# Kernel optimization log

Hardware: AMD Instinct MI355X
Metric: run time of the kernel (lower is better)

The kernel has to match this reference:

```python
import jax, jax.numpy as jnp
import numpy as np

LEAK = 0.95
THRESHOLD = 1.0
RESCALE = 2.0


def _xavier_uniform(key, shape, gain=2.0):
    fan_out, fan_in = shape
    bound = gain * np.sqrt(6.0 / (fan_in + fan_out))
    return jax.random.uniform(key, shape, jnp.float32, -bound, bound)


def setup_inputs() -> dict:
    key = jax.random.key(0)
    k_inp, k_w1, k_w2 = jax.random.split(key, 3)
    inp = jax.random.normal(k_inp, (8192, 784), jnp.float32)
    w1 = _xavier_uniform(k_w1, (800, 784))   # fc1.weight
    w2 = _xavier_uniform(k_w2, (10, 800))    # fc2.weight
    return {"inp": inp, "w1": w1, "w2": w2, "num_steps": 25}


@jax.custom_vjp
def spike_fn(x):
    return (x > 0).astype(x.dtype)

def _spike_fwd(x):
    return spike_fn(x), x

def _spike_bwd(x, g):
    # grad = g * 0.3 * relu(1 - |x|)  (surrogate BP)
    return (g * 0.3 * jnp.maximum(1.0 - jnp.abs(x), 0.0),)

spike_fn.defvjp(_spike_fwd, _spike_bwd)


def poisson_gen(key, inp):
    r = jax.random.uniform(key, inp.shape, inp.dtype)
    temp = (r * RESCALE <= jnp.abs(inp)).astype(inp.dtype) * jnp.sign(inp)
    return 0.5 * (temp + 1.0)


def reference(inp, w1, w2, num_steps):
    batch = inp.shape[0]
    x = inp.reshape(batch, -1)
    keys = jax.random.split(jax.random.key(42), num_steps)

    def step(carry, key):
        mem1, mem2 = carry
        sp = poisson_gen(key, x)                    # [B, 784]
        mem1 = LEAK * mem1 + (1.0 - LEAK) * (sp @ w1.T)  # [B, 800]
        mem_thr = mem1 / THRESHOLD - 1.0
        out = spike_fn(mem_thr)
        rst = jnp.where(mem_thr > 0, THRESHOLD, 0.0)
        mem1 = mem1 - jax.lax.stop_gradient(rst)
        mem2 = mem2 + out @ w2.T                    # [B, 10]
        return (mem1, mem2), None

    init = (jnp.zeros((batch, 800), x.dtype), jnp.zeros((batch, 10), x.dtype))
    (_, mem2), _ = jax.lax.scan(step, init, keys)
    return mem2 / num_steps
```

## Files before the change

kernel.cpp:

```cpp
#include <hip/hip_runtime.h>
#include <cstdint>

__host__ __device__ inline uint32_t tf_rotl32(uint32_t x, uint32_t r) {
  return (x << r) | (x >> (32u - r));
}

__host__ __device__ inline void threefry2x32(uint32_t k0, uint32_t k1,
                                             uint32_t x0, uint32_t x1,
                                             uint32_t* o0, uint32_t* o1) {
  uint32_t ks0 = k0, ks1 = k1, ks2 = k0 ^ k1 ^ 0x1BD11BDAu;
  x0 += ks0; x1 += ks1;
#define TF_R(r) { x0 += x1; x1 = tf_rotl32(x1, r); x1 ^= x0; }
  TF_R(13) TF_R(15) TF_R(26) TF_R(6)
  x0 += ks1; x1 += ks2 + 1u;
  TF_R(17) TF_R(29) TF_R(16) TF_R(24)
  x0 += ks2; x1 += ks0 + 2u;
  TF_R(13) TF_R(15) TF_R(26) TF_R(6)
  x0 += ks0; x1 += ks1 + 3u;
  TF_R(17) TF_R(29) TF_R(16) TF_R(24)
  x0 += ks1; x1 += ks2 + 4u;
  TF_R(13) TF_R(15) TF_R(26) TF_R(6)
  x0 += ks2; x1 += ks0 + 5u;
#undef TF_R
  *o0 = x0; *o1 = x1;
}

#define BSZ   8192
#define KIN   784
#define HID   800
#define NOUT  10
#define NSTEP 25

#define PANEL1 264
#define PANEL2 528

__global__ __launch_bounds__(256) void enc_kernel(const float* __restrict__ inp,
                                                  uint8_t* __restrict__ enc,
                                                  uint32_t k0, uint32_t k1) {
  int j = blockIdx.x * blockDim.x + threadIdx.x;
  if (j >= BSZ * KIN) return;
  uint32_t o0, o1;
  threefry2x32(k0, k1, 0u, (uint32_t)j, &o0, &o1);
  uint32_t bits = o0 ^ o1;
  float r = __uint_as_float((bits >> 9) | 0x3f800000u) - 1.0f;
  float x = inp[j];
  bool cond = (2.0f * r <= fabsf(x));
  int s = (x > 0.0f) ? 1 : ((x < 0.0f) ? -1 : 0);
  enc[j] = (uint8_t)(1 + (cond ? s : 0));
}

#define BM 128
#define BN 32
#define BK 16
#define NTILE (KIN / BK)

typedef float f32x2 __attribute__((ext_vector_type(2)));

__device__ __forceinline__ float cvt_ub(uint32_t x, int i) {
  return (float)((x >> (8 * i)) & 0xffu);
}

__device__ __forceinline__ void pk_fma_lo(f32x2& acc, f32x2 a, f32x2 b) {
  asm("v_pk_fma_f32 %0, %1, %2, %0 op_sel:[0,0,0] op_sel_hi:[0,1,1]"
      : "+v"(acc)
      : "v"(a), "v"(b));
}
__device__ __forceinline__ void pk_fma_hi(f32x2& acc, f32x2 a, f32x2 b) {
  asm("v_pk_fma_f32 %0, %1, %2, %0 op_sel:[1,0,0] op_sel_hi:[1,1,1]"
      : "+v"(acc)
      : "v"(a), "v"(b));
}

__global__ __launch_bounds__(256) void gemm_kernel(const uint8_t* __restrict__ enc,
                                                   const float* __restrict__ w1,
                                                   float* __restrict__ g) {
  __shared__ uint32_t As[2][BK][BM / 4];
  __shared__ float    Bs[2][BK][BN];
  const int m0 = blockIdx.x * BM;
  const int n0 = blockIdx.y * BN;
  const int t  = threadIdx.x;

  const int tm = t / 8;
  const int tn = t % 8;

  const bool isA = (t < 128);
  const int u    = t & 127;
  const int ar0  = (u & 31) * 4;
  const int ak0  = (u >> 5) * 4;
  const int brow = u & 31;
  const int bk0  = (u >> 5) * 4;

  const uint8_t* aptr = enc + (size_t)(m0 + ar0) * KIN + ak0;
  const float*   bptr = w1 + (size_t)(n0 + brow) * KIN + bk0;

  uint32_t rA0, rA1, rA2, rA3;
  float4 rB;

  f32x2 acc[4][2];
  f32x2 tot[4][2];
#pragma unroll
  for (int mi = 0; mi < 4; mi++)
#pragma unroll
    for (int nj = 0; nj < 2; nj++) acc[mi][nj] = (f32x2)(0.0f);

#define LOAD_TILE(K0G)                                               \
  if (isA) {                                                         \
    const uint8_t* ap = aptr + (K0G);                                \
    rA0 = *(const uint32_t*)(ap + (size_t)0 * KIN);                  \
    rA1 = *(const uint32_t*)(ap + (size_t)1 * KIN);                  \
    rA2 = *(const uint32_t*)(ap + (size_t)2 * KIN);                  \
    rA3 = *(const uint32_t*)(ap + (size_t)3 * KIN);                  \
  } else {                                                           \
    rB = *(const float4*)(bptr + (K0G));                             \
  }

#define STORE_TILE(P)                                                \
  if (isA) {                                                         \
    uint32_t a01  = __builtin_amdgcn_perm(rA1, rA0, 0x05010400u);    \
    uint32_t a01h = __builtin_amdgcn_perm(rA1, rA0, 0x07030602u);    \
    uint32_t a23  = __builtin_amdgcn_perm(rA3, rA2, 0x05010400u);    \
    uint32_t a23h = __builtin_amdgcn_perm(rA3, rA2, 0x07030602u);    \
    As[P][ak0 + 0][ar0 >> 2] = __builtin_amdgcn_perm(a23,  a01,  0x05040100u); \
    As[P][ak0 + 1][ar0 >> 2] = __builtin_amdgcn_perm(a23,  a01,  0x07060302u); \
    As[P][ak0 + 2][ar0 >> 2] = __builtin_amdgcn_perm(a23h, a01h, 0x05040100u); \
    As[P][ak0 + 3][ar0 >> 2] = __builtin_amdgcn_perm(a23h, a01h, 0x07060302u); \
  } else {                                                           \
    Bs[P][bk0 + 0][brow] = rB.x;                                     \
    Bs[P][bk0 + 1][brow] = rB.y;                                     \
    Bs[P][bk0 + 2][brow] = rB.z;                                     \
    Bs[P][bk0 + 3][brow] = rB.w;                                     \
  }

  LOAD_TILE(0)
  STORE_TILE(0)
  __syncthreads();

  int p = 0;
  for (int tile = 0; tile < NTILE; tile++) {
    const int kbase = tile * BK;
    const bool more = (tile + 1 < NTILE);
    if (more) { LOAD_TILE(kbase + BK) }
#pragma unroll
    for (int kk = 0; kk < BK; kk++) {
      const int kglob = kbase + kk;
      if (kglob == PANEL1) {
#pragma unroll
        for (int mi = 0; mi < 4; mi++)
#pragma unroll
          for (int nj = 0; nj < 2; nj++) {
            tot[mi][nj] = acc[mi][nj];
            acc[mi][nj] = (f32x2)(0.0f);
          }
      } else if (kglob == PANEL2) {
#pragma unroll
        for (int mi = 0; mi < 4; mi++)
#pragma unroll
          for (int nj = 0; nj < 2; nj++) {
            tot[mi][nj].x = __fadd_rn(tot[mi][nj].x, acc[mi][nj].x);
            tot[mi][nj].y = __fadd_rn(tot[mi][nj].y, acc[mi][nj].y);
            acc[mi][nj] = (f32x2)(0.0f);
          }
      }
      uint32_t aw = As[p][kk][tm];
      f32x2 am[2];
      am[0].x = cvt_ub(aw, 0);
      am[0].y = cvt_ub(aw, 1);
      am[1].x = cvt_ub(aw, 2);
      am[1].y = cvt_ub(aw, 3);
      float4 bv = *(const float4*)&Bs[p][kk][tn * 4];
      f32x2 b2[2];
      b2[0].x = bv.x; b2[0].y = bv.y;
      b2[1].x = bv.z; b2[1].y = bv.w;
#pragma unroll
      for (int mp = 0; mp < 2; mp++) {
        pk_fma_lo(acc[2 * mp + 0][0], am[mp], b2[0]);
        pk_fma_lo(acc[2 * mp + 0][1], am[mp], b2[1]);
        pk_fma_hi(acc[2 * mp + 1][0], am[mp], b2[0]);
        pk_fma_hi(acc[2 * mp + 1][1], am[mp], b2[1]);
      }
    }
    if (more) { STORE_TILE(p ^ 1) }
    __syncthreads();
    p ^= 1;
  }
#undef LOAD_TILE
#undef STORE_TILE

#pragma unroll
  for (int mi = 0; mi < 4; mi++) {
    float* dst = g + (size_t)(m0 + tm * 4 + mi) * HID + n0 + tn * 4;
    float4 o;
    o.x = __fmul_rn(0.5f, __fadd_rn(tot[mi][0].x, acc[mi][0].x));
    o.y = __fmul_rn(0.5f, __fadd_rn(tot[mi][0].y, acc[mi][0].y));
    o.z = __fmul_rn(0.5f, __fadd_rn(tot[mi][1].x, acc[mi][1].x));
    o.w = __fmul_rn(0.5f, __fadd_rn(tot[mi][1].y, acc[mi][1].y));
    *(float4*)dst = o;
  }
}

__global__ __launch_bounds__(256) void update_kernel(const float* __restrict__ g,
                                                     float* __restrict__ mem1,
                                                     const float* __restrict__ w2,
                                                     float* __restrict__ mem2) {
  __shared__ float w2s[NOUT * HID];
  for (int i = threadIdx.x; i < NOUT * HID; i += 256) w2s[i] = w2[i];
  __syncthreads();

  const int wave = threadIdx.x / 64;
  const int lane = threadIdx.x % 64;
  const int b = blockIdx.x * 4 + wave;

  const float* grow = g + (size_t)b * HID;
  float* mrow = mem1 + (size_t)b * HID;

  float acc[NOUT];
#pragma unroll
  for (int i = 0; i < NOUT; i++) acc[i] = 0.0f;

  for (int j = lane; j < HID; j += 64) {
    float m = __fadd_rn(__fmul_rn(0.95f, mrow[j]), __fmul_rn(0.05f, grow[j]));
    bool spike = __fadd_rn(m, -1.0f) > 0.0f;
    mrow[j] = spike ? __fadd_rn(m, -1.0f) : m;
    if (spike) {
#pragma unroll
      for (int i = 0; i < NOUT; i++) acc[i] += w2s[i * HID + j];
    }
  }
#pragma unroll
  for (int i = 0; i < NOUT; i++) {
    float v = acc[i];
    for (int off = 32; off > 0; off >>= 1) v += __shfl_down(v, off);
    if (lane == 0) mem2[(size_t)b * NOUT + i] += v;
  }
}

__global__ __launch_bounds__(256) void finalize_kernel(const float* __restrict__ mem2,
                                                       const int* __restrict__ ns,
                                                       float* __restrict__ out) {
  int i = blockIdx.x * blockDim.x + threadIdx.x;
  if (i < BSZ * NOUT) out[i] = mem2[i] / (float)(*ns);
}

extern "C" void kernel_launch(void* const* d_in, const int* in_sizes, int n_in,
                              void* d_out, int out_size, void* d_ws, size_t ws_size,
                              hipStream_t stream) {
  const float* inp = (const float*)d_in[0];
  const float* w1  = (const float*)d_in[1];
  const float* w2  = (const float*)d_in[2];
  const int*   dns = (const int*)d_in[3];
  float* out = (float*)d_out;

  char* ws = (char*)d_ws;
  size_t off = 0;
  uint8_t* enc = (uint8_t*)(ws + off);  off += (size_t)BSZ * KIN;
  off = (off + 255) & ~(size_t)255;
  float* g    = (float*)(ws + off);     off += (size_t)BSZ * HID * 4;
  float* mem1 = (float*)(ws + off);     off += (size_t)BSZ * HID * 4;
  float* mem2 = (float*)(ws + off);     off += (size_t)BSZ * NOUT * 4;

  (void)hipMemsetAsync(mem1, 0, (size_t)BSZ * HID * 4, stream);
  (void)hipMemsetAsync(mem2, 0, (size_t)BSZ * NOUT * 4, stream);

  uint32_t keys[NSTEP][2];
  for (int t = 0; t < NSTEP; t++)
    threefry2x32(0u, 42u, 0u, (uint32_t)t, &keys[t][0], &keys[t][1]);

  const int n_elem = BSZ * KIN;
  for (int t = 0; t < NSTEP; t++) {
    enc_kernel<<<(n_elem + 255) / 256, 256, 0, stream>>>(inp, enc, keys[t][0], keys[t][1]);
    gemm_kernel<<<dim3(BSZ / BM, HID / BN), 256, 0, stream>>>(enc, w1, g);
    update_kernel<<<BSZ / 4, 256, 0, stream>>>(g, mem1, w2, mem2);
  }
  finalize_kernel<<<(BSZ * NOUT + 255) / 256, 256, 0, stream>>>(mem2, dns, out);
}
```

Before: 4.754 ms.

## Split GEMM K dimension into three panels across grid z and reduce in update

The GEMM now launches three times as many blocks, each covering one of three K panels (264/264/256) with BK reduced to 8. Each block writes its partial sums to a separate buffer, and the update kernel adds the three partials and applies the 0.5 scale. This keeps the same panel summation order as the old kernel, which chained the panels sequentially inside one block, while exposing more parallelism. The cost is triple the intermediate write and read traffic (about 26 MB per partial per step) and smaller K tiles with more barriers per element.

```diff
diff --git a/kernel.cpp b/kernel.cpp
--- a/kernel.cpp
+++ b/kernel.cpp
@@ -31,8 +31,6 @@
 #define NOUT  10
 #define NSTEP 25
 
-#define PANEL1 264
-#define PANEL2 528
 
 __global__ __launch_bounds__(256) void enc_kernel(const float* __restrict__ inp,
                                                   uint8_t* __restrict__ enc,
@@ -51,8 +49,7 @@
 
 #define BM 128
 #define BN 32
-#define BK 16
-#define NTILE (KIN / BK)
+#define BK 8
 
 typedef float f32x2 __attribute__((ext_vector_type(2)));
 
@@ -73,9 +70,12 @@
 
 __global__ __launch_bounds__(256) void gemm_kernel(const uint8_t* __restrict__ enc,
                                                    const float* __restrict__ w1,
-                                                   float* __restrict__ g) {
+                                                   float* __restrict__ gp) {
   __shared__ uint32_t As[2][BK][BM / 4];
   __shared__ float    Bs[2][BK][BN];
+  const int panel  = blockIdx.z;
+  const int kstart = (panel == 0) ? 0 : ((panel == 1) ? 264 : 528);
+  const int ntile  = (panel == 2) ? 32 : 33;
   const int m0 = blockIdx.x * BM;
   const int n0 = blockIdx.y * BN;
   const int t  = threadIdx.x;
@@ -83,52 +83,56 @@
   const int tm = t / 8;
   const int tn = t % 8;
 
-  const bool isA = (t < 128);
-  const int u    = t & 127;
-  const int ar0  = (u & 31) * 4;
-  const int ak0  = (u >> 5) * 4;
-  const int brow = u & 31;
-  const int bk0  = (u >> 5) * 4;
-
-  const uint8_t* aptr = enc + (size_t)(m0 + ar0) * KIN + ak0;
-  const float*   bptr = w1 + (size_t)(n0 + brow) * KIN + bk0;
+  const bool stA = (t < 64);
+  const bool stB = (t >= 128 && t < 192);
+  const int ar0 = (t & 31) * 4;
+  const int ak0 = ((t >> 5) & 1) * 4;
+  const int ub   = (t - 128) & 63;
+  const int brow = ub & 31;
+  const int bk0  = (ub >> 5) * 4;
+
+  const uint8_t* aptr = enc + (size_t)(m0 + ar0) * KIN + kstart + ak0;
+  const float*   bptr = w1 + (size_t)(n0 + brow) * KIN + kstart + bk0;
 
   uint32_t rA0, rA1, rA2, rA3;
   float4 rB;
 
   f32x2 acc[4][2];
-  f32x2 tot[4][2];
 #pragma unroll
   for (int mi = 0; mi < 4; mi++)
 #pragma unroll
     for (int nj = 0; nj < 2; nj++) acc[mi][nj] = (f32x2)(0.0f);
 
-#define LOAD_TILE(K0G)                                               \
-  if (isA) {                                                         \
-    const uint8_t* ap = aptr + (K0G);                                \
-    rA0 = *(const uint32_t*)(ap + (size_t)0 * KIN);                  \
-    rA1 = *(const uint32_t*)(ap + (size_t)1 * KIN);                  \
-    rA2 = *(const uint32_t*)(ap + (size_t)2 * KIN);                  \
-    rA3 = *(const uint32_t*)(ap + (size_t)3 * KIN);                  \
-  } else {                                                           \
-    rB = *(const float4*)(bptr + (K0G));                             \
+#define LOAD_TILE(KOFF)                                              \
+  {                                                                  \
+    if (stA) {                                                       \
+      const uint8_t* ap = aptr + (KOFF);                             \
+      rA0 = *(const uint32_t*)(ap + (size_t)0 * KIN);                \
+      rA1 = *(const uint32_t*)(ap + (size_t)1 * KIN);                \
+      rA2 = *(const uint32_t*)(ap + (size_t)2 * KIN);                \
+      rA3 = *(const uint32_t*)(ap + (size_t)3 * KIN);                \
+    }                                                                \
+    if (stB) rB = *(const float4*)(bptr + (KOFF));                   \
   }
 
 #define STORE_TILE(P)                                                \
-  if (isA) {                                                         \
-    uint32_t a01  = __builtin_amdgcn_perm(rA1, rA0, 0x05010400u);    \
-    uint32_t a01h = __builtin_amdgcn_perm(rA1, rA0, 0x07030602u);    \
-    uint32_t a23  = __builtin_amdgcn_perm(rA3, rA2, 0x05010400u);    \
-    uint32_t a23h = __builtin_amdgcn_perm(rA3, rA2, 0x07030602u);    \
-    As[P][ak0 + 0][ar0 >> 2] = __builtin_amdgcn_perm(a23,  a01,  0x05040100u); \
-    As[P][ak0 + 1][ar0 >> 2] = __builtin_amdgcn_perm(a23,  a01,  0x07060302u); \
-    As[P][ak0 + 2][ar0 >> 2] = __builtin_amdgcn_perm(a23h, a01h, 0x05040100u); \
-    As[P][ak0 + 3][ar0 >> 2] = __builtin_amdgcn_perm(a23h, a01h, 0x07060302u); \
-  } else {                                                           \
-    Bs[P][bk0 + 0][brow] = rB.x;                                     \
-    Bs[P][bk0 + 1][brow] = rB.y;                                     \
-    Bs[P][bk0 + 2][brow] = rB.z;                                     \
-    Bs[P][bk0 + 3][brow] = rB.w;                                     \
+  {                                                                  \
+    if (stA) {                                                       \
+      uint32_t a01  = __builtin_amdgcn_perm(rA1, rA0, 0x05010400u);  \
+      uint32_t a01h = __builtin_amdgcn_perm(rA1, rA0, 0x07030602u);  \
+      uint32_t a23  = __builtin_amdgcn_perm(rA3, rA2, 0x05010400u);  \
+      uint32_t a23h = __builtin_amdgcn_perm(rA3, rA2, 0x07030602u);  \
+      As[P][ak0 + 0][ar0 >> 2] = __builtin_amdgcn_perm(a23,  a01,  0x05040100u); \
+      As[P][ak0 + 1][ar0 >> 2] = __builtin_amdgcn_perm(a23,  a01,  0x07060302u); \
+      As[P][ak0 + 2][ar0 >> 2] = __builtin_amdgcn_perm(a23h, a01h, 0x05040100u); \
+      As[P][ak0 + 3][ar0 >> 2] = __builtin_amdgcn_perm(a23h, a01h, 0x07060302u); \
+    }                                                                \
+    if (stB) {                                                       \
+      Bs[P][bk0 + 0][brow] = rB.x;                                   \
+      Bs[P][bk0 + 1][brow] = rB.y;                                   \
+      Bs[P][bk0 + 2][brow] = rB.z;                                   \
+      Bs[P][bk0 + 3][brow] = rB.w;                                   \
+    }                                                                \
   }
 
   LOAD_TILE(0)
@@ -136,47 +140,29 @@
   __syncthreads();
 
   int p = 0;
-  for (int tile = 0; tile < NTILE; tile++) {
-    const int kbase = tile * BK;
-    const bool more = (tile + 1 < NTILE);
-    if (more) { LOAD_TILE(kbase + BK) }
-#pragma unroll
-    for (int kk = 0; kk < BK; kk++) {
-      const int kglob = kbase + kk;
-      if (kglob == PANEL1) {
-#pragma unroll
-        for (int mi = 0; mi < 4; mi++)
-#pragma unroll
-          for (int nj = 0; nj < 2; nj++) {
-            tot[mi][nj] = acc[mi][nj];
-            acc[mi][nj] = (f32x2)(0.0f);
-          }
-      } else if (kglob == PANEL2) {
-#pragma unroll
-        for (int mi = 0; mi < 4; mi++)
-#pragma unroll
-          for (int nj = 0; nj < 2; nj++) {
-            tot[mi][nj].x = __fadd_rn(tot[mi][nj].x, acc[mi][nj].x);
-            tot[mi][nj].y = __fadd_rn(tot[mi][nj].y, acc[mi][nj].y);
-            acc[mi][nj] = (f32x2)(0.0f);
-          }
-      }
-      uint32_t aw = As[p][kk][tm];
-      f32x2 am[2];
-      am[0].x = cvt_ub(aw, 0);
-      am[0].y = cvt_ub(aw, 1);
-      am[1].x = cvt_ub(aw, 2);
-      am[1].y = cvt_ub(aw, 3);
-      float4 bv = *(const float4*)&Bs[p][kk][tn * 4];
-      f32x2 b2[2];
-      b2[0].x = bv.x; b2[0].y = bv.y;
-      b2[1].x = bv.z; b2[1].y = bv.w;
-#pragma unroll
-      for (int mp = 0; mp < 2; mp++) {
-        pk_fma_lo(acc[2 * mp + 0][0], am[mp], b2[0]);
-        pk_fma_lo(acc[2 * mp + 0][1], am[mp], b2[1]);
-        pk_fma_hi(acc[2 * mp + 1][0], am[mp], b2[0]);
-        pk_fma_hi(acc[2 * mp + 1][1], am[mp], b2[1]);
+  for (int tile = 0; tile < ntile; tile++) {
+    const bool more = (tile + 1 < ntile);
+    if (more) { LOAD_TILE((size_t)(tile + 1) * BK) }
+    {
+      const uint32_t* arow = &As[p][0][tm];
+      const float*    brw  = &Bs[p][0][tn * 4];
+#pragma unroll
+      for (int kk = 0; kk < BK; kk++) {
+        uint32_t aw = arow[(size_t)kk * (BM / 4)];
+        float4 bv = *(const float4*)(brw + (size_t)kk * BN);
+        f32x2 am[2];
+        am[0].x = cvt_ub(aw, 0); am[0].y = cvt_ub(aw, 1);
+        am[1].x = cvt_ub(aw, 2); am[1].y = cvt_ub(aw, 3);
+        f32x2 b2[2];
+        b2[0].x = bv.x; b2[0].y = bv.y;
+        b2[1].x = bv.z; b2[1].y = bv.w;
+#pragma unroll
+        for (int mp = 0; mp < 2; mp++) {
+          pk_fma_lo(acc[2 * mp + 0][0], am[mp], b2[0]);
+          pk_fma_lo(acc[2 * mp + 0][1], am[mp], b2[1]);
+          pk_fma_hi(acc[2 * mp + 1][0], am[mp], b2[0]);
+          pk_fma_hi(acc[2 * mp + 1][1], am[mp], b2[1]);
+        }
       }
     }
     if (more) { STORE_TILE(p ^ 1) }
@@ -186,19 +172,20 @@
 #undef LOAD_TILE
 #undef STORE_TILE
 
+  float* base = gp + (size_t)panel * BSZ * HID;
 #pragma unroll
   for (int mi = 0; mi < 4; mi++) {
-    float* dst = g + (size_t)(m0 + tm * 4 + mi) * HID + n0 + tn * 4;
+    float* dst = base + (size_t)(m0 + tm * 4 + mi) * HID + n0 + tn * 4;
     float4 o;
-    o.x = __fmul_rn(0.5f, __fadd_rn(tot[mi][0].x, acc[mi][0].x));
-    o.y = __fmul_rn(0.5f, __fadd_rn(tot[mi][0].y, acc[mi][0].y));
-    o.z = __fmul_rn(0.5f, __fadd_rn(tot[mi][1].x, acc[mi][1].x));
-    o.w = __fmul_rn(0.5f, __fadd_rn(tot[mi][1].y, acc[mi][1].y));
+    o.x = acc[mi][0].x;
+    o.y = acc[mi][0].y;
+    o.z = acc[mi][1].x;
+    o.w = acc[mi][1].y;
     *(float4*)dst = o;
   }
 }
 
-__global__ __launch_bounds__(256) void update_kernel(const float* __restrict__ g,
+__global__ __launch_bounds__(256) void update_kernel(const float* __restrict__ gp,
                                                      float* __restrict__ mem1,
                                                      const float* __restrict__ w2,
                                                      float* __restrict__ mem2) {
@@ -210,7 +197,10 @@
   const int lane = threadIdx.x % 64;
   const int b = blockIdx.x * 4 + wave;
 
-  const float* grow = g + (size_t)b * HID;
+  const size_t GS = (size_t)BSZ * HID;
+  const float* g0 = gp + (size_t)b * HID;
+  const float* g1 = g0 + GS;
+  const float* g2 = g1 + GS;
   float* mrow = mem1 + (size_t)b * HID;
 
   float acc[NOUT];
@@ -218,7 +208,8 @@
   for (int i = 0; i < NOUT; i++) acc[i] = 0.0f;
 
   for (int j = lane; j < HID; j += 64) {
-    float m = __fadd_rn(__fmul_rn(0.95f, mrow[j]), __fmul_rn(0.05f, grow[j]));
+    float gs = __fmul_rn(0.5f, __fadd_rn(__fadd_rn(g0[j], g1[j]), g2[j]));
+    float m = __fadd_rn(__fmul_rn(0.95f, mrow[j]), __fmul_rn(0.05f, gs));
     bool spike = __fadd_rn(m, -1.0f) > 0.0f;
     mrow[j] = spike ? __fadd_rn(m, -1.0f) : m;
     if (spike) {
@@ -254,7 +245,7 @@
   size_t off = 0;
   uint8_t* enc = (uint8_t*)(ws + off);  off += (size_t)BSZ * KIN;
   off = (off + 255) & ~(size_t)255;
-  float* g    = (float*)(ws + off);     off += (size_t)BSZ * HID * 4;
+  float* gp   = (float*)(ws + off);     off += (size_t)3 * BSZ * HID * 4;
   float* mem1 = (float*)(ws + off);     off += (size_t)BSZ * HID * 4;
   float* mem2 = (float*)(ws + off);     off += (size_t)BSZ * NOUT * 4;
 
@@ -268,8 +259,8 @@
   const int n_elem = BSZ * KIN;
   for (int t = 0; t < NSTEP; t++) {
     enc_kernel<<<(n_elem + 255) / 256, 256, 0, stream>>>(inp, enc, keys[t][0], keys[t][1]);
-    gemm_kernel<<<dim3(BSZ / BM, HID / BN), 256, 0, stream>>>(enc, w1, g);
-    update_kernel<<<BSZ / 4, 256, 0, stream>>>(g, mem1, w2, mem2);
+    gemm_kernel<<<dim3(BSZ / BM, HID / BN, 3), 256, 0, stream>>>(enc, w1, gp);
+    update_kernel<<<BSZ / 4, 256, 0, stream>>>(gp, mem1, w2, mem2);
   }
   finalize_kernel<<<(BSZ * NOUT + 255) / 256, 256, 0, stream>>>(mem2, dns, out);
 }
```

New measurement: 4.681 ms. Within noise of the previous version (-1.6%).
